# Optimization experiments

Measured on AMD Instinct MI355X. Metric: run time of the kernel, lower is better.

Reference implementation:

```python
import jax, jax.numpy as jnp
import numpy as np

B, T, I, H, O = 64, 256, 512, 1024, 512


def setup_inputs() -> dict:
    key = jax.random.key(0)
    ks = jax.random.split(key, 12)
    s_i, s_h = 1.0 / np.sqrt(H), 1.0 / np.sqrt(H)  # torch nn.RNN init scale U(-1/sqrt(H), 1/sqrt(H)); use scaled normal
    return {
        "x": jax.random.normal(ks[0], (B, T, I), dtype=jnp.float32),
        "h0": jnp.zeros((B, H), dtype=jnp.float32),
        "W_ih1": jax.random.normal(ks[1], (H, I), dtype=jnp.float32) * s_i,
        "W_hh1": jax.random.normal(ks[2], (H, H), dtype=jnp.float32) * s_h,
        "b_ih1": jax.random.normal(ks[3], (H,), dtype=jnp.float32) * s_h,
        "b_hh1": jax.random.normal(ks[4], (H,), dtype=jnp.float32) * s_h,
        "W_ih2": jax.random.normal(ks[5], (H, H), dtype=jnp.float32) * s_h,
        "W_hh2": jax.random.normal(ks[6], (H, H), dtype=jnp.float32) * s_h,
        "b_ih2": jax.random.normal(ks[7], (H,), dtype=jnp.float32) * s_h,
        "b_hh2": jax.random.normal(ks[8], (H,), dtype=jnp.float32) * s_h,
        "W_fc": jax.random.normal(ks[9], (O, H), dtype=jnp.float32) * s_h,
        "b_fc": jax.random.normal(ks[10], (O,), dtype=jnp.float32) * s_h,
    }


def _rnn_tanh_layer(x_seq, h0, W_ih, W_hh, b_ih, b_hh):
    """Single-layer tanh RNN, batch_first. x_seq:[B,T,I], h0:[B,H] -> (outs:[B,T,H], h_last:[B,H])."""
    xw = jnp.einsum("bti,hi->bth", x_seq, W_ih) + b_ih  # precompute input projection

    def step(h, xw_t):  # xw_t: [B,H]
        h = jnp.tanh(xw_t + h @ W_hh.T + b_hh)
        return h, h

    h_last, ys = jax.lax.scan(step, h0, jnp.swapaxes(xw, 0, 1))  # scan over T
    return jnp.swapaxes(ys, 0, 1), h_last


def reference(x, h0, W_ih1, W_hh1, b_ih1, b_hh1, W_ih2, W_hh2, b_ih2, b_hh2, W_fc, b_fc):
    out1, h1 = _rnn_tanh_layer(x, h0, W_ih1, W_hh1, b_ih1, b_hh1)
    # Faithful to original: rnn2's initial hidden is rnn1's FINAL hidden (hidden1)
    out2, h2 = _rnn_tanh_layer(out1, h1, W_ih2, W_hh2, b_ih2, b_hh2)
    logits = out2[:, -1, :] @ W_fc.T + b_fc  # [B,O]
    probs = jax.nn.softmax(logits, axis=-1)
    return probs, h2
```

## Files before the change

### kernel.cpp

```cpp
#include <hip/hip_runtime.h>

#define NB 64
#define NT 256
#define NI 512
#define NH 1024
#define NO 512

typedef _Float16 half8 __attribute__((ext_vector_type(8)));
typedef _Float16 half4 __attribute__((ext_vector_type(4)));
typedef float    f32x4 __attribute__((ext_vector_type(4)));

union H8 { half8 v; unsigned long long u[2]; };
union H4 { half4 v; unsigned long long u; };

#define OFF_W1   (32u * 1024u * 1024u)
#define OFF_W2   (OFF_W1 + 1u * 1024u * 1024u)
#define OFF_WH1  (OFF_W2 + 2u * 1024u * 1024u)
#define OFF_WH2  (OFF_WH1 + 2u * 1024u * 1024u)
#define OFF_HBUF (OFF_WH2 + 2u * 1024u * 1024u)
#define OFF_SLOT (OFF_HBUF + 256u * 1024u)

#define XF4 2097152u

__device__ __forceinline__ unsigned ald32(const unsigned* p) {
    return __hip_atomic_load(p, __ATOMIC_RELAXED, __HIP_MEMORY_SCOPE_AGENT);
}
__device__ __forceinline__ void ast32(unsigned* p, unsigned v) {
    __hip_atomic_store(p, v, __ATOMIC_RELAXED, __HIP_MEMORY_SCOPE_AGENT);
}
__device__ __forceinline__ unsigned long long ald64(const void* p) {
    return __hip_atomic_load((const unsigned long long*)p,
                             __ATOMIC_RELAXED, __HIP_MEMORY_SCOPE_AGENT);
}
__device__ __forceinline__ void ast64(void* p, unsigned long long v) {
    __hip_atomic_store((unsigned long long*)p, v,
                       __ATOMIC_RELAXED, __HIP_MEMORY_SCOPE_AGENT);
}
__device__ __forceinline__ half8 load_h8(const _Float16* p) {
    H8 r;
    r.u[0] = ald64(p);
    r.u[1] = ald64(p + 4);
    return r.v;
}

__device__ __forceinline__ float tanh_fast(float z) {
    const float e = __expf(2.0f * z);
    return 1.0f - 2.0f * __builtin_amdgcn_rcpf(e + 1.0f);
}

__global__ void k_init(const float* __restrict__ h0,
                       const float* __restrict__ Wih1, const float* __restrict__ Wih2,
                       const float* __restrict__ Whh1, const float* __restrict__ Whh2,
                       _Float16* __restrict__ hb0, _Float16* __restrict__ w1,
                       _Float16* __restrict__ w2, _Float16* __restrict__ wh1,
                       _Float16* __restrict__ wh2, unsigned* __restrict__ slots)
{
    const int i = blockIdx.x * 256 + threadIdx.x;
    if (i < NB * NH) hb0[i] = (_Float16)h0[i];
    if (i < NH * NI) w1[i] = (_Float16)Wih1[i];
    if (i < NH * NH) {
        w2[i]  = (_Float16)Wih2[i];
        wh1[i] = (_Float16)Whh1[i];
        wh2[i] = (_Float16)Whh2[i];
    }
    if (i < 512) slots[i] = 0u;
}

#define MFMA4(A, W, base)                                                                     \
    ac0 = __builtin_amdgcn_mfma_f32_16x16x32_f16((A)[(base)+0], (W)[(base)+0], ac0, 0, 0, 0); \
    ac1 = __builtin_amdgcn_mfma_f32_16x16x32_f16((A)[(base)+1], (W)[(base)+1], ac1, 0, 0, 0); \
    ac2 = __builtin_amdgcn_mfma_f32_16x16x32_f16((A)[(base)+2], (W)[(base)+2], ac2, 0, 0, 0); \
    ac3 = __builtin_amdgcn_mfma_f32_16x16x32_f16((A)[(base)+3], (W)[(base)+3], ac3, 0, 0, 0);

#define POLL_WAIT(tgt)                                                                        \
    {                                                                                         \
        const unsigned tgt_ = (unsigned)(tgt);                                                \
        while (true) {                                                                        \
            const unsigned v_ = ald32(gs + lane);                                             \
            if (__all((int)(v_ >= tgt_))) break;                                              \
        }                                                                                     \
        asm volatile("" ::: "memory");                                                        \
    }

#define LOAD_SHARE(hbase)                                                                     \
    {                                                                                         \
        const _Float16* const s_ = (hbase) + (size_t)(g16 + shr) * NH + wv * 256 + shc * 64;  \
        half8 q_[8];                                                                          \
        _Pragma("unroll")                                                                     \
        for (int i_ = 0; i_ < 8; ++i_) q_[i_] = load_h8(s_ + i_ * 8);                         \
        _Float16* const d_ = &hsh[shr][wv * 256 + shc * 64];                                  \
        _Pragma("unroll")                                                                     \
        for (int i_ = 0; i_ < 8; ++i_) *(half8*)(d_ + i_ * 8) = q_[i_];                       \
    }

#define REC_MFMA                                                                              \
    {                                                                                         \
        half8 ahh[32];                                                                        \
        _Pragma("unroll")                                                                     \
        for (int c = 0; c < 32; ++c)                                                          \
            ahh[c] = *(const half8*)&hsh[row][c * 32 + quad * 8];                             \
        MFMA4(ahh, whh, 0)  MFMA4(ahh, whh, 4)  MFMA4(ahh, whh, 8)  MFMA4(ahh, whh, 12)      \
        MFMA4(ahh, whh, 16) MFMA4(ahh, whh, 20) MFMA4(ahh, whh, 24) MFMA4(ahh, whh, 28)      \
    }

#define PRE_P0(t_)                                                                            \
    {                                                                                         \
        const float*    const xb_ = x  + ((size_t)brow * NT + (t_)) * NI + quad * 8;          \
        const _Float16* const wb_ = w1 + (size_t)nglb * NI + quad * 8;                        \
        ac0 = (f32x4){0.f, 0.f, 0.f, 0.f}; ac1 = ac0; ac2 = ac0; ac3 = ac0;                   \
        _Pragma("unroll")                                                                     \
        for (int c = 0; c < 16; c += 4) {                                                     \
            const f32x4* q0 = (const f32x4*)(xb_ + (c + 0) * 32);                             \
            const f32x4* q1 = (const f32x4*)(xb_ + (c + 1) * 32);                             \
            const f32x4* q2 = (const f32x4*)(xb_ + (c + 2) * 32);                             \
            const f32x4* q3 = (const f32x4*)(xb_ + (c + 3) * 32);                             \
            half8 a0, a1, a2, a3;                                                             \
            _Pragma("unroll")                                                                 \
            for (int e = 0; e < 4; ++e) {                                                     \
                a0[e] = (_Float16)q0[0][e]; a0[e + 4] = (_Float16)q0[1][e];                   \
                a1[e] = (_Float16)q1[0][e]; a1[e + 4] = (_Float16)q1[1][e];                   \
                a2[e] = (_Float16)q2[0][e]; a2[e + 4] = (_Float16)q2[1][e];                   \
                a3[e] = (_Float16)q3[0][e]; a3[e + 4] = (_Float16)q3[1][e];                   \
            }                                                                                 \
            half8 b0 = *(const half8*)(wb_ + (c + 0) * 32);                                   \
            half8 b1 = *(const half8*)(wb_ + (c + 1) * 32);                                   \
            half8 b2 = *(const half8*)(wb_ + (c + 2) * 32);                                   \
            half8 b3 = *(const half8*)(wb_ + (c + 3) * 32);                                   \
            ac0 = __builtin_amdgcn_mfma_f32_16x16x32_f16(a0, b0, ac0, 0, 0, 0);               \
            ac1 = __builtin_amdgcn_mfma_f32_16x16x32_f16(a1, b1, ac1, 0, 0, 0);               \
            ac2 = __builtin_amdgcn_mfma_f32_16x16x32_f16(a2, b2, ac2, 0, 0, 0);               \
            ac3 = __builtin_amdgcn_mfma_f32_16x16x32_f16(a3, b3, ac3, 0, 0, 0);               \
        }                                                                                     \
    }

#define PRE_P1(t_)                                                                            \
    {                                                                                         \
        const _Float16* const ob_ = out1 + ((size_t)(t_) * NB + brow) * NH + quad * 8;        \
        const _Float16* const wb_ = w2 + (size_t)nglb * NH + quad * 8;                        \
        ac0 = (f32x4){0.f, 0.f, 0.f, 0.f}; ac1 = ac0; ac2 = ac0; ac3 = ac0;                   \
        _Pragma("unroll")                                                                     \
        for (int c = 0; c < 32; c += 4) {                                                     \
            half8 a0 = *(const half8*)(ob_ + (c + 0) * 32);                                   \
            half8 a1 = *(const half8*)(ob_ + (c + 1) * 32);                                   \
            half8 a2 = *(const half8*)(ob_ + (c + 2) * 32);                                   \
            half8 a3 = *(const half8*)(ob_ + (c + 3) * 32);                                   \
            half8 b0 = *(const half8*)(wb_ + (c + 0) * 32);                                   \
            half8 b1 = *(const half8*)(wb_ + (c + 1) * 32);                                   \
            half8 b2 = *(const half8*)(wb_ + (c + 2) * 32);                                   \
            half8 b3 = *(const half8*)(wb_ + (c + 3) * 32);                                   \
            ac0 = __builtin_amdgcn_mfma_f32_16x16x32_f16(a0, b0, ac0, 0, 0, 0);               \
            ac1 = __builtin_amdgcn_mfma_f32_16x16x32_f16(a1, b1, ac1, 0, 0, 0);               \
            ac2 = __builtin_amdgcn_mfma_f32_16x16x32_f16(a2, b2, ac2, 0, 0, 0);               \
            ac3 = __builtin_amdgcn_mfma_f32_16x16x32_f16(a3, b3, ac3, 0, 0, 0);               \
        }                                                                                     \
    }

#define SIGNAL(val)                                                                           \
    {                                                                                         \
        asm volatile("s_waitcnt vmcnt(0)" ::: "memory");                                      \
        if (lane == 0) ast32(gs + myslot, (unsigned)(val));                                   \
    }

__launch_bounds__(256, 1)
__global__ void k_scan(const float* __restrict__ x,
                       const _Float16* __restrict__ wh1,
                       const _Float16* __restrict__ wh2,
                       const float* __restrict__ bih1, const float* __restrict__ bhh1,
                       const float* __restrict__ bih2, const float* __restrict__ bhh2,
                       const _Float16* __restrict__ w1,
                       const _Float16* __restrict__ w2,
                       _Float16* __restrict__ out1,
                       _Float16* __restrict__ hbuf,
                       float* __restrict__ h2out,
                       unsigned* __restrict__ slots)
{
    const int bid = blockIdx.x;

    if (bid >= 192) {
        const unsigned* flag = slots + 508;
        const f32x4* base = (const f32x4*)x;
        float acc = 0.f;
        unsigned off = (unsigned)(bid - 192) * 32768u;
        while (ald32(flag) == 0u) {
            #pragma unroll
            for (int it = 0; it < 32; ++it) {
                const unsigned idx = (off + (unsigned)it * 256u + (unsigned)threadIdx.x)
                                     & (XF4 - 1u);
                const f32x4 v = __builtin_nontemporal_load(base + idx);
                acc += v[0] + v[1] + v[2] + v[3];
            }
            off += 32u * 256u;
        }
        if (acc == 1234.567f) ((volatile float*)slots)[509] = acc;
        return;
    }
    if (bid >= 64) {
        const unsigned* flag = slots + 508;
        float a0 = 1.0f, a1 = 1.1f, a2 = 1.2f, a3 = 1.3f;
        const float b = 1.0000001f;
        while (ald32(flag) == 0u) {
            #pragma unroll 32
            for (int i = 0; i < 512; ++i) {
                asm volatile("v_fmac_f32 %0, %1, %2" : "+v"(a0) : "v"(b), "v"(a1));
                asm volatile("v_fmac_f32 %0, %1, %2" : "+v"(a1) : "v"(b), "v"(a2));
                asm volatile("v_fmac_f32 %0, %1, %2" : "+v"(a2) : "v"(b), "v"(a3));
                asm volatile("v_fmac_f32 %0, %1, %2" : "+v"(a3) : "v"(b), "v"(a0));
            }
        }
        if (a0 == 1234.567f) ((volatile float*)slots)[510] = a0;
        return;
    }

    __shared__ alignas(16) _Float16 tile[4][16][20];
    __shared__ alignas(16) _Float16 hsh[16][NH + 4];

    const int tid  = threadIdx.x;
    const int wv   = tid >> 6;
    const int lane = tid & 63;
    const int quad = lane >> 4;
    const int row  = lane & 15;
    const int g    = bid & 3;
    const int g16  = g << 4;
    const int j    = bid >> 2;
    const int n0   = j * 64 + wv * 16;
    const int nglb = n0 + row;
    const int brow = g16 + row;
    const int shr  = lane >> 2;
    const int shc  = lane & 3;
    const int myslot = j * 4 + wv;
    unsigned* const gs = slots + g * 64;

    half8 whh[32];
    f32x4 ac0, ac1, ac2, ac3;

    #pragma unroll
    for (int c = 0; c < 32; ++c)
        whh[c] = *(const half8*)(wh1 + (size_t)nglb * NH + c * 32 + quad * 8);
    float bias = bih1[nglb] + bhh1[nglb];

    PRE_P0(0)
    for (int t = 0; t < NT; ++t) {
        const int r = t;
        if (r > 0) POLL_WAIT(r)

        LOAD_SHARE(hbuf + (size_t)(r & 1) * (NB * NH))
        __syncthreads();
        REC_MFMA

        f32x4 z;
        #pragma unroll
        for (int e = 0; e < 4; ++e) z[e] = ac0[e] + ac1[e] + ac2[e] + ac3[e] + bias;
        half4 tv;
        #pragma unroll
        for (int e = 0; e < 4; ++e) tv[e] = (_Float16)tanh_fast(z[e]);
        *(half4*)&tile[wv][row][quad * 4] = tv;
        H4 pk;
        pk.v[0] = tile[wv][quad * 4 + 0][row];
        pk.v[1] = tile[wv][quad * 4 + 1][row];
        pk.v[2] = tile[wv][quad * 4 + 2][row];
        pk.v[3] = tile[wv][quad * 4 + 3][row];
        const int bg = g16 + row;
        const int nc = n0 + quad * 4;

        ast64(hbuf + (size_t)((r + 1) & 1) * (NB * NH) + (size_t)bg * NH + nc, pk.u);
        SIGNAL(r + 1)
        ast64(out1 + ((size_t)t * NB + bg) * NH + nc, pk.u);

        if (t + 1 < NT) PRE_P0(t + 1)
    }

    #pragma unroll
    for (int c = 0; c < 32; ++c)
        whh[c] = *(const half8*)(wh2 + (size_t)nglb * NH + c * 32 + quad * 8);
    bias = bih2[nglb] + bhh2[nglb];

    PRE_P1(0)
    for (int t = 0; t < NT; ++t) {
        const int r = NT + t;
        POLL_WAIT(r)

        LOAD_SHARE(hbuf + (size_t)(r & 1) * (NB * NH))
        __syncthreads();
        REC_MFMA

        f32x4 z;
        #pragma unroll
        for (int e = 0; e < 4; ++e) z[e] = ac0[e] + ac1[e] + ac2[e] + ac3[e] + bias;
        half4 tv;
        #pragma unroll
        for (int e = 0; e < 4; ++e) tv[e] = (_Float16)tanh_fast(z[e]);
        *(half4*)&tile[wv][row][quad * 4] = tv;
        H4 pk;
        pk.v[0] = tile[wv][quad * 4 + 0][row];
        pk.v[1] = tile[wv][quad * 4 + 1][row];
        pk.v[2] = tile[wv][quad * 4 + 2][row];
        pk.v[3] = tile[wv][quad * 4 + 3][row];
        const int bg = g16 + row;
        const int nc = n0 + quad * 4;

        if (r != 2 * NT - 1) {
            ast64(hbuf + (size_t)((r + 1) & 1) * (NB * NH) + (size_t)bg * NH + nc, pk.u);
            SIGNAL(r + 1)
            PRE_P1(t + 1)
        } else {
            f32x4 fo;
            fo[0] = (float)pk.v[0]; fo[1] = (float)pk.v[1];
            fo[2] = (float)pk.v[2]; fo[3] = (float)pk.v[3];
            *(f32x4*)(h2out + (size_t)bg * NH + nc) = fo;
        }
    }

    if (bid == 0 && tid == 0) ast32(slots + 508, 1u);
}

__global__ void k_fc(const float* __restrict__ h2, const float* __restrict__ Wfc,
                     const float* __restrict__ bfc, float* __restrict__ probs)
{
    __shared__ float hrow[NH];
    __shared__ float logits[NO];
    __shared__ float red[8];

    const int b = blockIdx.x;
    const int tid = threadIdx.x;
    const int wave = tid >> 6;
    const int lane = tid & 63;

    for (int i = tid; i < NH; i += 256) hrow[i] = h2[b * NH + i];
    __syncthreads();

    float hl[16];
    #pragma unroll
    for (int e = 0; e < 16; ++e) hl[e] = hrow[lane * 16 + e];

    for (int o = wave * 128; o < wave * 128 + 128; ++o) {
        const float* wr = Wfc + o * NH + lane * 16;
        float s = 0.f;
        #pragma unroll
        for (int e = 0; e < 16; ++e) s += hl[e] * wr[e];
        #pragma unroll
        for (int off = 32; off > 0; off >>= 1) s += __shfl_down(s, off, 64);
        if (lane == 0) logits[o] = s + bfc[o];
    }
    __syncthreads();

    float m = -1e30f;
    for (int o = tid; o < NO; o += 256) m = fmaxf(m, logits[o]);
    #pragma unroll
    for (int off = 32; off > 0; off >>= 1) m = fmaxf(m, __shfl_down(m, off, 64));
    if (lane == 0) red[wave] = m;
    __syncthreads();
    const float mx = fmaxf(fmaxf(red[0], red[1]), fmaxf(red[2], red[3]));

    float sum = 0.f;
    for (int o = tid; o < NO; o += 256) sum += expf(logits[o] - mx);
    #pragma unroll
    for (int off = 32; off > 0; off >>= 1) sum += __shfl_down(sum, off, 64);
    if (lane == 0) red[4 + wave] = sum;
    __syncthreads();
    const float inv = 1.f / (red[4] + red[5] + red[6] + red[7]);

    for (int o = tid; o < NO; o += 256) probs[b * NO + o] = expf(logits[o] - mx) * inv;
}

extern "C" void kernel_launch(void* const* d_in, const int* in_sizes, int n_in,
                              void* d_out, int out_size, void* d_ws, size_t ws_size,
                              hipStream_t stream)
{
    const float* x    = (const float*)d_in[0];
    const float* h0   = (const float*)d_in[1];
    const float* Wih1 = (const float*)d_in[2];
    const float* Whh1 = (const float*)d_in[3];
    const float* bih1 = (const float*)d_in[4];
    const float* bhh1 = (const float*)d_in[5];
    const float* Wih2 = (const float*)d_in[6];
    const float* Whh2 = (const float*)d_in[7];
    const float* bih2 = (const float*)d_in[8];
    const float* bhh2 = (const float*)d_in[9];
    const float* Wfc  = (const float*)d_in[10];
    const float* bfc  = (const float*)d_in[11];

    float* outp  = (float*)d_out;
    float* h2out = outp + NB * NO;

    char* ws = (char*)d_ws;
    _Float16* out1 = (_Float16*)ws;
    _Float16* w1   = (_Float16*)(ws + OFF_W1);
    _Float16* w2   = (_Float16*)(ws + OFF_W2);
    _Float16* wh1  = (_Float16*)(ws + OFF_WH1);
    _Float16* wh2  = (_Float16*)(ws + OFF_WH2);
    _Float16* hbuf = (_Float16*)(ws + OFF_HBUF);
    unsigned* slots= (unsigned*)(ws + OFF_SLOT);

    hipLaunchKernelGGL(k_init, dim3(4096), dim3(256), 0, stream,
                       h0, Wih1, Wih2, Whh1, Whh2, hbuf, w1, w2, wh1, wh2, slots);

    hipLaunchKernelGGL(k_scan, dim3(256), dim3(256), 0, stream,
                       x, wh1, wh2, bih1, bhh1, bih2, bhh2,
                       w1, w2, out1, hbuf, h2out, slots);

    hipLaunchKernelGGL(k_fc, dim3(NB), dim3(256), 0, stream, h2out, Wfc, bfc, outp);
}
```

Measured before the change: 5.385 ms.

## Pin each batch group to one XCD and use sc0 cache-scoped sync loads/stores

Work groups now read their XCD id at startup and are assigned dynamically, so the 16 blocks that share a batch group (and exchange hidden state every step) all sit on the same XCD. Four such groups get real work and the rest become the existing load/ALU filler blocks. Hidden-state exchange and flag polling switch from agent-scope atomics to inline-asm global loads and stores with sc0, which should keep the traffic in the XCD-local L2 instead of going to device-coherent memory. This depends on sc0 coherence holding within one XCD and on enough blocks landing per XCD, and the assignment handshake adds spinning at startup.

```diff
diff --git a/kernel.cpp b/kernel.cpp
--- a/kernel.cpp
+++ b/kernel.cpp
@@ -10,7 +10,6 @@
 typedef _Float16 half4 __attribute__((ext_vector_type(4)));
 typedef float    f32x4 __attribute__((ext_vector_type(4)));
 
-union H8 { half8 v; unsigned long long u[2]; };
 union H4 { half4 v; unsigned long long u; };
 
 #define OFF_W1   (32u * 1024u * 1024u)
@@ -19,8 +18,12 @@
 #define OFF_WH2  (OFF_WH1 + 2u * 1024u * 1024u)
 #define OFF_HBUF (OFF_WH2 + 2u * 1024u * 1024u)
 #define OFF_SLOT (OFF_HBUF + 256u * 1024u)
+#define OFF_CTL  (OFF_SLOT + 4096u)
 
 #define XF4 2097152u
+
+#define UNSET 0xFFFFFFFFu
+#define BAL   0xFFFFFFFEu
 
 __device__ __forceinline__ unsigned ald32(const unsigned* p) {
     return __hip_atomic_load(p, __ATOMIC_RELAXED, __HIP_MEMORY_SCOPE_AGENT);
@@ -28,19 +31,37 @@
 __device__ __forceinline__ void ast32(unsigned* p, unsigned v) {
     __hip_atomic_store(p, v, __ATOMIC_RELAXED, __HIP_MEMORY_SCOPE_AGENT);
 }
-__device__ __forceinline__ unsigned long long ald64(const void* p) {
-    return __hip_atomic_load((const unsigned long long*)p,
-                             __ATOMIC_RELAXED, __HIP_MEMORY_SCOPE_AGENT);
-}
-__device__ __forceinline__ void ast64(void* p, unsigned long long v) {
-    __hip_atomic_store((unsigned long long*)p, v,
-                       __ATOMIC_RELAXED, __HIP_MEMORY_SCOPE_AGENT);
-}
-__device__ __forceinline__ half8 load_h8(const _Float16* p) {
-    H8 r;
-    r.u[0] = ald64(p);
-    r.u[1] = ald64(p + 4);
-    return r.v;
+
+__device__ __forceinline__ void st8_sc0(void* p, unsigned long long v) {
+    asm volatile("global_store_dwordx2 %0, %1, off sc0\n\t"
+                 "s_waitcnt vmcnt(0)" :: "v"(p), "v"(v) : "memory");
+}
+__device__ __forceinline__ void st4_sc0(void* p, unsigned v) {
+    asm volatile("global_store_dword %0, %1, off sc0\n\t"
+                 "s_waitcnt vmcnt(0)" :: "v"(p), "v"(v) : "memory");
+}
+__device__ __forceinline__ unsigned ld4_sc0(const void* p) {
+    unsigned r;
+    asm volatile("global_load_dword %0, %1, off sc0\n\t"
+                 "s_waitcnt vmcnt(0)" : "=&v"(r) : "v"(p) : "memory");
+    return r;
+}
+__device__ __forceinline__ void ld128_sc0(const void* p,
+        f32x4& q0, f32x4& q1, f32x4& q2, f32x4& q3,
+        f32x4& q4, f32x4& q5, f32x4& q6, f32x4& q7) {
+    asm volatile(
+        "global_load_dwordx4 %0, %8, off sc0\n\t"
+        "global_load_dwordx4 %1, %8, off offset:16 sc0\n\t"
+        "global_load_dwordx4 %2, %8, off offset:32 sc0\n\t"
+        "global_load_dwordx4 %3, %8, off offset:48 sc0\n\t"
+        "global_load_dwordx4 %4, %8, off offset:64 sc0\n\t"
+        "global_load_dwordx4 %5, %8, off offset:80 sc0\n\t"
+        "global_load_dwordx4 %6, %8, off offset:96 sc0\n\t"
+        "global_load_dwordx4 %7, %8, off offset:112 sc0\n\t"
+        "s_waitcnt vmcnt(0)"
+        : "=&v"(q0), "=&v"(q1), "=&v"(q2), "=&v"(q3),
+          "=&v"(q4), "=&v"(q5), "=&v"(q6), "=&v"(q7)
+        : "v"(p) : "memory");
 }
 
 __device__ __forceinline__ float tanh_fast(float z) {
@@ -53,7 +74,8 @@
                        const float* __restrict__ Whh1, const float* __restrict__ Whh2,
                        _Float16* __restrict__ hb0, _Float16* __restrict__ w1,
                        _Float16* __restrict__ w2, _Float16* __restrict__ wh1,
-                       _Float16* __restrict__ wh2, unsigned* __restrict__ slots)
+                       _Float16* __restrict__ wh2, unsigned* __restrict__ slots,
+                       unsigned* __restrict__ ctl)
 {
     const int i = blockIdx.x * 256 + threadIdx.x;
     if (i < NB * NH) hb0[i] = (_Float16)h0[i];
@@ -64,6 +86,7 @@
         wh2[i] = (_Float16)Whh2[i];
     }
     if (i < 512) slots[i] = 0u;
+    if (i < 144) ctl[i] = (i >= 16) ? UNSET : 0u;
 }
 
 #define MFMA4(A, W, base)                                                                     \
@@ -76,21 +99,19 @@
     {                                                                                         \
         const unsigned tgt_ = (unsigned)(tgt);                                                \
         while (true) {                                                                        \
-            const unsigned v_ = ald32(gs + lane);                                             \
+            const unsigned v_ = ld4_sc0(gs + lane);                                           \
             if (__all((int)(v_ >= tgt_))) break;                                              \
         }                                                                                     \
-        asm volatile("" ::: "memory");                                                        \
     }
 
 #define LOAD_SHARE(hbase)                                                                     \
     {                                                                                         \
         const _Float16* const s_ = (hbase) + (size_t)(g16 + shr) * NH + wv * 256 + shc * 64;  \
-        half8 q_[8];                                                                          \
-        _Pragma("unroll")                                                                     \
-        for (int i_ = 0; i_ < 8; ++i_) q_[i_] = load_h8(s_ + i_ * 8);                         \
-        _Float16* const d_ = &hsh[shr][wv * 256 + shc * 64];                                  \
-        _Pragma("unroll")                                                                     \
-        for (int i_ = 0; i_ < 8; ++i_) *(half8*)(d_ + i_ * 8) = q_[i_];                       \
+        f32x4 q0, q1, q2, q3, q4, q5, q6, q7;                                                 \
+        ld128_sc0(s_, q0, q1, q2, q3, q4, q5, q6, q7);                                        \
+        f32x4* const d_ = (f32x4*)&hsh[shr][wv * 256 + shc * 64];                             \
+        d_[0] = q0; d_[1] = q1; d_[2] = q2; d_[3] = q3;                                       \
+        d_[4] = q4; d_[5] = q5; d_[6] = q6; d_[7] = q7;                                       \
     }
 
 #define REC_MFMA                                                                              \
@@ -156,10 +177,7 @@
     }
 
 #define SIGNAL(val)                                                                           \
-    {                                                                                         \
-        asm volatile("s_waitcnt vmcnt(0)" ::: "memory");                                      \
-        if (lane == 0) ast32(gs + myslot, (unsigned)(val));                                   \
-    }
+    { if (lane == 0) st4_sc0(gs + myslot, (unsigned)(val)); }
 
 __launch_bounds__(256, 1)
 __global__ void k_scan(const float* __restrict__ x,
@@ -172,56 +190,82 @@
                        _Float16* __restrict__ out1,
                        _Float16* __restrict__ hbuf,
                        float* __restrict__ h2out,
-                       unsigned* __restrict__ slots)
+                       unsigned* __restrict__ slots,
+                       unsigned* __restrict__ ctl)
 {
-    const int bid = blockIdx.x;
-
-    if (bid >= 192) {
-        const unsigned* flag = slots + 508;
-        const f32x4* base = (const f32x4*)x;
-        float acc = 0.f;
-        unsigned off = (unsigned)(bid - 192) * 32768u;
-        while (ald32(flag) == 0u) {
-            #pragma unroll
-            for (int it = 0; it < 32; ++it) {
-                const unsigned idx = (off + (unsigned)it * 256u + (unsigned)threadIdx.x)
-                                     & (XF4 - 1u);
-                const f32x4 v = __builtin_nontemporal_load(base + idx);
-                acc += v[0] + v[1] + v[2] + v[3];
-            }
-            off += 32u * 256u;
-        }
-        if (acc == 1234.567f) ((volatile float*)slots)[509] = acc;
-        return;
-    }
-    if (bid >= 64) {
-        const unsigned* flag = slots + 508;
-        float a0 = 1.0f, a1 = 1.1f, a2 = 1.2f, a3 = 1.3f;
-        const float b = 1.0000001f;
-        while (ald32(flag) == 0u) {
-            #pragma unroll 32
-            for (int i = 0; i < 512; ++i) {
-                asm volatile("v_fmac_f32 %0, %1, %2" : "+v"(a0) : "v"(b), "v"(a1));
-                asm volatile("v_fmac_f32 %0, %1, %2" : "+v"(a1) : "v"(b), "v"(a2));
-                asm volatile("v_fmac_f32 %0, %1, %2" : "+v"(a2) : "v"(b), "v"(a3));
-                asm volatile("v_fmac_f32 %0, %1, %2" : "+v"(a3) : "v"(b), "v"(a0));
+    __shared__ alignas(16) _Float16 tile[4][16][20];
+    __shared__ alignas(16) _Float16 hsh[16][NH + 4];
+    __shared__ unsigned sh_m, sh_pos;
+
+    const int tid = threadIdx.x;
+
+    unsigned xcd;
+    asm volatile("s_getreg_b32 %0, hwreg(HW_REG_XCC_ID)" : "=s"(xcd));
+    xcd &= 7u;
+    if (tid == 0) {
+        const unsigned rank = atomicAdd(&ctl[xcd], 1u);
+        __hip_atomic_fetch_add(&ctl[8], 1u, __ATOMIC_RELEASE, __HIP_MEMORY_SCOPE_AGENT);
+        const unsigned set = rank >> 4, pos = rank & 15u;
+        unsigned* const mp = &ctl[16 + xcd * 16u + set];
+        unsigned m;
+        if (pos == 15u) {
+            const unsigned gi = atomicAdd(&ctl[9], 1u);
+            m = (gi < 4u) ? gi : BAL;
+            __hip_atomic_store(mp, m, __ATOMIC_RELEASE, __HIP_MEMORY_SCOPE_AGENT);
+        } else {
+            while ((m = ald32(mp)) == UNSET) {
+                if (__hip_atomic_load(&ctl[8], __ATOMIC_ACQUIRE, __HIP_MEMORY_SCOPE_AGENT)
+                        >= 256u &&
+                    ald32(&ctl[xcd]) <= set * 16u + 15u) { m = BAL; break; }
+                __builtin_amdgcn_s_sleep(8);
             }
         }
-        if (a0 == 1234.567f) ((volatile float*)slots)[510] = a0;
+        sh_m = m; sh_pos = pos;
+    }
+    __syncthreads();
+    const unsigned m = sh_m;
+
+    if (m >= 4u) {
+        const unsigned* flag = slots + 508;
+        if (blockIdx.x & 1) {
+            const f32x4* base = (const f32x4*)x;
+            float acc = 0.f;
+            unsigned off = (unsigned)blockIdx.x * 16384u;
+            while (ald32(flag) == 0u) {
+                #pragma unroll
+                for (int it = 0; it < 32; ++it) {
+                    const unsigned idx = (off + (unsigned)it * 256u + (unsigned)tid)
+                                         & (XF4 - 1u);
+                    const f32x4 v = __builtin_nontemporal_load(base + idx);
+                    acc += v[0] + v[1] + v[2] + v[3];
+                }
+                off += 32u * 256u;
+            }
+            if (acc == 1234.567f) ((volatile float*)slots)[509] = acc;
+        } else {
+            float a0 = 1.0f, a1 = 1.1f, a2 = 1.2f, a3 = 1.3f;
+            const float b = 1.0000001f;
+            while (ald32(flag) == 0u) {
+                #pragma unroll 32
+                for (int i = 0; i < 512; ++i) {
+                    asm volatile("v_fmac_f32 %0, %1, %2" : "+v"(a0) : "v"(b), "v"(a1));
+                    asm volatile("v_fmac_f32 %0, %1, %2" : "+v"(a1) : "v"(b), "v"(a2));
+                    asm volatile("v_fmac_f32 %0, %1, %2" : "+v"(a2) : "v"(b), "v"(a3));
+                    asm volatile("v_fmac_f32 %0, %1, %2" : "+v"(a3) : "v"(b), "v"(a0));
+                }
+            }
+            if (a0 == 1234.567f) ((volatile float*)slots)[510] = a0;
+        }
         return;
     }
 
-    __shared__ alignas(16) _Float16 tile[4][16][20];
-    __shared__ alignas(16) _Float16 hsh[16][NH + 4];
-
-    const int tid  = threadIdx.x;
+    const int g    = (int)m;
+    const int j    = (int)sh_pos;
     const int wv   = tid >> 6;
     const int lane = tid & 63;
     const int quad = lane >> 4;
     const int row  = lane & 15;
-    const int g    = bid & 3;
     const int g16  = g << 4;
-    const int j    = bid >> 2;
     const int n0   = j * 64 + wv * 16;
     const int nglb = n0 + row;
     const int brow = g16 + row;
@@ -262,9 +306,9 @@
         const int bg = g16 + row;
         const int nc = n0 + quad * 4;
 
-        ast64(hbuf + (size_t)((r + 1) & 1) * (NB * NH) + (size_t)bg * NH + nc, pk.u);
+        st8_sc0(hbuf + (size_t)((r + 1) & 1) * (NB * NH) + (size_t)bg * NH + nc, pk.u);
         SIGNAL(r + 1)
-        ast64(out1 + ((size_t)t * NB + bg) * NH + nc, pk.u);
+        st8_sc0(out1 + ((size_t)t * NB + bg) * NH + nc, pk.u);
 
         if (t + 1 < NT) PRE_P0(t + 1)
     }
@@ -299,7 +343,7 @@
         const int nc = n0 + quad * 4;
 
         if (r != 2 * NT - 1) {
-            ast64(hbuf + (size_t)((r + 1) & 1) * (NB * NH) + (size_t)bg * NH + nc, pk.u);
+            st8_sc0(hbuf + (size_t)((r + 1) & 1) * (NB * NH) + (size_t)bg * NH + nc, pk.u);
             SIGNAL(r + 1)
             PRE_P1(t + 1)
         } else {
@@ -310,7 +354,7 @@
         }
     }
 
-    if (bid == 0 && tid == 0) ast32(slots + 508, 1u);
+    if (j == 0 && tid == 0) ast32(slots + 508, 1u);
 }
 
 __global__ void k_fc(const float* __restrict__ h2, const float* __restrict__ Wfc,
@@ -343,11 +387,11 @@
     }
     __syncthreads();
 
-    float m = -1e30f;
-    for (int o = tid; o < NO; o += 256) m = fmaxf(m, logits[o]);
+    float mx0 = -1e30f;
+    for (int o = tid; o < NO; o += 256) mx0 = fmaxf(mx0, logits[o]);
     #pragma unroll
-    for (int off = 32; off > 0; off >>= 1) m = fmaxf(m, __shfl_down(m, off, 64));
-    if (lane == 0) red[wave] = m;
+    for (int off = 32; off > 0; off >>= 1) mx0 = fmaxf(mx0, __shfl_down(mx0, off, 64));
+    if (lane == 0) red[wave] = mx0;
     __syncthreads();
     const float mx = fmaxf(fmaxf(red[0], red[1]), fmaxf(red[2], red[3]));
 
@@ -390,13 +434,14 @@
     _Float16* wh2  = (_Float16*)(ws + OFF_WH2);
     _Float16* hbuf = (_Float16*)(ws + OFF_HBUF);
     unsigned* slots= (unsigned*)(ws + OFF_SLOT);
+    unsigned* ctl  = (unsigned*)(ws + OFF_CTL);
 
     hipLaunchKernelGGL(k_init, dim3(4096), dim3(256), 0, stream,
-                       h0, Wih1, Wih2, Whh1, Whh2, hbuf, w1, w2, wh1, wh2, slots);
+                       h0, Wih1, Wih2, Whh1, Whh2, hbuf, w1, w2, wh1, wh2, slots, ctl);
 
     hipLaunchKernelGGL(k_scan, dim3(256), dim3(256), 0, stream,
                        x, wh1, wh2, bih1, bhh1, bih2, bhh2,
-                       w1, w2, out1, hbuf, h2out, slots);
+                       w1, w2, out1, hbuf, h2out, slots, ctl);
 
     hipLaunchKernelGGL(k_fc, dim3(NB), dim3(256), 0, stream, h2out, Wfc, bfc, outp);
 }
```

Measured after the change: 4.981 ms. 7.5% less time.
